# Performance work log

Hardware: AMD Instinct MI355X
Metric: run time of the kernel (lower is better)

Reference implementation:

```python
import jax, jax.numpy as jnp
import numpy as np

NUM_HEADS = 12
ROPE_THETA = 10000.0


def _rope_cos_sin(n, hd, dtype):
    inv_freq = 1.0 / (ROPE_THETA ** (np.arange(0, hd, 2, dtype=np.float64) / hd))
    freqs = np.outer(np.arange(n, dtype=np.float64), inv_freq)  # (N, hd/2)
    emb = np.concatenate([freqs, freqs], axis=-1)               # (N, hd)
    return jnp.asarray(np.cos(emb), dtype), jnp.asarray(np.sin(emb), dtype)


def _apply_rope(t, cos, sin):
    # t: (B, H, N, hd); rotate-half convention
    half = t.shape[-1] // 2
    t1, t2 = t[..., :half], t[..., half:]
    rot = jnp.concatenate([-t2, t1], axis=-1)
    return t * cos + rot * sin


def setup_inputs() -> dict:
    key = jax.random.key(0)
    k1, k2, k3 = jax.random.split(key, 3)
    B, N, C = 8, 1024, 768
    x = jax.random.normal(k1, (B, N, C), dtype=jnp.float32)
    w_qkv = jax.random.normal(k2, (C, 3 * C), dtype=jnp.float32) * 0.02
    w_proj = jax.random.normal(k3, (C, C), dtype=jnp.float32) * 0.02
    b_proj = jnp.zeros((C,), dtype=jnp.float32)
    return {"x": x, "w_qkv": w_qkv, "w_proj": w_proj, "b_proj": b_proj}


def reference(x, w_qkv, w_proj, b_proj):
    B, N, C = x.shape
    H = NUM_HEADS
    hd = C // H
    scale = hd ** -0.5
    # qkv: (B,N,3C) -> (B,N,3,H,hd) -> (B,H,3,N,hd)
    qkv = (x @ w_qkv).reshape(B, N, 3, H, hd).transpose(0, 3, 2, 1, 4)
    q, k, v = qkv[:, :, 0], qkv[:, :, 1], qkv[:, :, 2]  # each (B,H,N,hd)
    cos, sin = _rope_cos_sin(N, hd, x.dtype)
    q = _apply_rope(q, cos, sin)
    k = _apply_rope(k, cos, sin)
    attn = jax.nn.softmax(jnp.einsum("bhqd,bhkd->bhqk", q, k) * scale, axis=-1)
    out = jnp.einsum("bhqk,bhkd->bhqd", attn, v)  # (B,H,N,hd)
    out = out.transpose(0, 2, 1, 3).reshape(B, N, C)
    return out @ w_proj + b_proj
```

## Files before the change

kernel.cpp:

```cpp
#include <hip/hip_runtime.h>

typedef unsigned short ushort_t;
typedef __bf16 bf16x8 __attribute__((ext_vector_type(8)));
typedef float f32x4 __attribute__((ext_vector_type(4)));
typedef unsigned short u16x8 __attribute__((ext_vector_type(8)));
typedef unsigned int u32x2 __attribute__((ext_vector_type(2)));

#define MFMA16(a, b, c) __builtin_amdgcn_mfma_f32_16x16x32_bf16((a), (b), (c), 0, 0, 0)

#define SEQ 1024
#define NHEAD 12
#define HD 64
#define CDIM 768
#define TS 6291456
#define QSCALE 0.1803368801111204f

__device__ __forceinline__ ushort_t f2bf(float f) {
  __bf16 b = (__bf16)f;
  return __builtin_bit_cast(ushort_t, b);
}
__device__ __forceinline__ unsigned pk2(float lo, float hi) {
  return (unsigned)f2bf(lo) | ((unsigned)f2bf(hi) << 16);
}
__device__ __forceinline__ float bf2f(ushort_t h) {
  return __builtin_bit_cast(float, ((unsigned int)h) << 16);
}

typedef __attribute__((address_space(1))) void gvoid_t;
typedef __attribute__((address_space(3))) void lvoid_t;
__device__ __forceinline__ void async16(const ushort_t* g, ushort_t* l) {
  __builtin_amdgcn_global_load_lds((gvoid_t*)g, (lvoid_t*)l, 16, 0, 0);
}

__device__ __forceinline__ void transpose_body(const float* __restrict__ in,
                                               ushort_t* __restrict__ out,
                                               int R, int C, int bxi, int byi,
                                               float (*tile)[33]) {
  int bx = bxi * 32, by = byi * 32;
  int tx = threadIdx.x & 31, ty = threadIdx.x >> 5;
#pragma unroll
  for (int i = ty; i < 32; i += 8) {
    int r = by + i, c = bx + tx;
    if (r < R && c < C) tile[i][tx] = in[(size_t)r * C + c];
  }
  __syncthreads();
#pragma unroll
  for (int i = ty; i < 32; i += 8) {
    int r = bx + i, c = by + tx;
    if (r < C && c < R) out[(size_t)r * R + c] = f2bf(tile[tx][i]);
  }
}

__global__ void __launch_bounds__(256) prep_all(const float* __restrict__ x,
                                                const float* __restrict__ w_qkv,
                                                const float* __restrict__ w_proj,
                                                ushort_t* __restrict__ xb,
                                                ushort_t* __restrict__ wqkvT,
                                                ushort_t* __restrict__ wprojT,
                                                float* __restrict__ tab) {
  __shared__ float tile[32][33];
  const int bid = blockIdx.x;
  if (bid < 3072) {
    int i = (bid * 256 + threadIdx.x) * 8;
    float4 a = *(const float4*)(x + i);
    float4 b = *(const float4*)(x + i + 4);
    u16x8 r;
    r[0] = f2bf(a.x); r[1] = f2bf(a.y); r[2] = f2bf(a.z); r[3] = f2bf(a.w);
    r[4] = f2bf(b.x); r[5] = f2bf(b.y); r[6] = f2bf(b.z); r[7] = f2bf(b.w);
    *(u16x8*)(xb + i) = r;
  } else if (bid < 3072 + 1728) {
    int t = bid - 3072;
    transpose_body(w_qkv, wqkvT, 768, 2304, t % 72, t / 72, tile);
  } else if (bid < 3072 + 1728 + 576) {
    int t = bid - (3072 + 1728);
    transpose_body(w_proj, wprojT, 768, 768, t % 24, t / 24, tile);
  } else {
    int g = (bid - 5376) * 256 + threadIdx.x;
    int n = g >> 5, j = g & 31;
    double invf = pow(10000.0, -((double)(2 * j)) / 64.0);
    double fr = (double)n * invf;
    tab[g * 2]     = (float)cos(fr);
    tab[g * 2 + 1] = (float)sin(fr);
  }
}

__device__ __forceinline__ void gemm_bt_core(const ushort_t* __restrict__ A,
                                             const ushort_t* __restrict__ Bt,
                                             int K, int bm, int bn,
                                             ushort_t* ldsA, ushort_t* ldsB,
                                             f32x4 acc[4][4]) {
  const int tid = threadIdx.x;
  const int lane = tid & 63, wid = tid >> 6;
  const int wm = (wid >> 1) * 64, wn = (wid & 1) * 64;
  const int fr = lane & 15, fq = lane >> 4;
#pragma unroll
  for (int i = 0; i < 4; ++i)
#pragma unroll
    for (int j = 0; j < 4; ++j) acc[i][j] = (f32x4){0.f, 0.f, 0.f, 0.f};

  const int srow = tid >> 2;
  const int scol = (tid & 3) * 8;
  const size_t aOff = (size_t)(bm + srow) * K + scol;
  const size_t bOff = (size_t)(bn + srow) * K + scol;

  for (int kt = 0; kt < K; kt += 32) {
    async16(A + aOff + kt, ldsA + tid * 8);
    async16(A + aOff + (size_t)64 * K + kt, ldsA + 2048 + tid * 8);
    async16(Bt + bOff + kt, ldsB + tid * 8);
    async16(Bt + bOff + (size_t)64 * K + kt, ldsB + 2048 + tid * 8);
    __syncthreads();
    bf16x8 aF[4], bF[4];
#pragma unroll
    for (int i = 0; i < 4; ++i)
      aF[i] = *(const bf16x8*)(ldsA + (wm + i * 16 + fr) * 32 + fq * 8);
#pragma unroll
    for (int j = 0; j < 4; ++j)
      bF[j] = *(const bf16x8*)(ldsB + (wn + j * 16 + fr) * 32 + fq * 8);
#pragma unroll
    for (int i = 0; i < 4; ++i)
#pragma unroll
      for (int j = 0; j < 4; ++j) acc[i][j] = MFMA16(aF[i], bF[j], acc[i][j]);
    __syncthreads();
  }
}

__global__ void __launch_bounds__(256) gemm_qkv(const ushort_t* __restrict__ A,
                                                const ushort_t* __restrict__ Bt,
                                                const float* __restrict__ tab,
                                                ushort_t* __restrict__ qkv) {
  __shared__ __attribute__((aligned(16))) ushort_t ldsA[4096];
  __shared__ __attribute__((aligned(16))) ushort_t ldsB[4096];
  f32x4 acc[4][4];
  const int bm = blockIdx.y * 128, bn = blockIdx.x * 128;
  gemm_bt_core(A, Bt, CDIM, bm, bn, ldsA, ldsB, acc);
  const int lane = threadIdx.x & 63, wid = threadIdx.x >> 6;
  const int wm = (wid >> 1) * 64, wn = (wid & 1) * 64;
  const int fr = lane & 15, fq = lane >> 4;
  const int tensor = bn / 768;

  if (tensor < 2) {
    ushort_t* dstT = qkv + (size_t)tensor * TS;
    const float qs = (tensor == 0) ? QSCALE : 1.0f;
#pragma unroll
    for (int i = 0; i < 4; ++i) {
#pragma unroll
      for (int jp = 0; jp < 2; ++jp) {
        const int col = bn + wn + jp * 16 + fr;
        const int rem = col - tensor * 768;
        const int h = rem >> 6;
        const int d2 = rem & 31;
#pragma unroll
        for (int rr = 0; rr < 4; ++rr) {
          const int row = bm + wm + i * 16 + fq * 4 + rr;
          const int b = row >> 10, n = row & 1023;
          const float2 cs = ((const float2*)tab)[n * 32 + d2];
          const float av = acc[i][jp][rr], bv = acc[i][jp + 2][rr];
          const float o1 = (av * cs.x - bv * cs.y) * qs;
          const float o2 = (bv * cs.x + av * cs.y) * qs;
          ushort_t* dst = dstT + ((size_t)(b * NHEAD + h) * SEQ + n) * HD + d2;
          dst[0]  = f2bf(o1);
          dst[32] = f2bf(o2);
        }
      }
    }
  } else {
    ushort_t* vt = qkv + 2 * (size_t)TS;
#pragma unroll
    for (int i = 0; i < 4; ++i) {
      const int row0 = bm + wm + i * 16 + fq * 4;
      const int b = row0 >> 10, n0 = row0 & 1023;
#pragma unroll
      for (int j = 0; j < 4; ++j) {
        const int col = bn + wn + j * 16 + fr;
        const int rem = col - 1536;
        const int h = rem >> 6, d = rem & 63;
        u32x2 pk;
        pk[0] = pk2(acc[i][j][0], acc[i][j][1]);
        pk[1] = pk2(acc[i][j][2], acc[i][j][3]);
        *(u32x2*)(vt + ((size_t)(b * NHEAD + h) * HD + d) * SEQ + n0) = pk;
      }
    }
  }
}

__global__ void __launch_bounds__(256) gemm_proj(const ushort_t* __restrict__ A,
                                                 const ushort_t* __restrict__ Bt,
                                                 const float* __restrict__ bias,
                                                 float* __restrict__ Cout) {
  __shared__ __attribute__((aligned(16))) ushort_t ldsA[4096];
  __shared__ __attribute__((aligned(16))) ushort_t ldsB[4096];
  f32x4 acc[4][4];
  const int bm = blockIdx.y * 128, bn = blockIdx.x * 128;
  gemm_bt_core(A, Bt, CDIM, bm, bn, ldsA, ldsB, acc);
  const int lane = threadIdx.x & 63, wid = threadIdx.x >> 6;
  const int wm = (wid >> 1) * 64, wn = (wid & 1) * 64;
  const int fr = lane & 15, fq = lane >> 4;
#pragma unroll
  for (int i = 0; i < 4; ++i) {
#pragma unroll
    for (int j = 0; j < 4; ++j) {
      const int col = bn + wn + j * 16 + fr;
      const float bv = bias[col];
#pragma unroll
      for (int rr = 0; rr < 4; ++rr) {
        const int row = bm + wm + i * 16 + fq * 4 + rr;
        Cout[(size_t)row * CDIM + col] = acc[i][j][rr] + bv;
      }
    }
  }
}

__global__ void __launch_bounds__(256, 3) attn_fused(const ushort_t* __restrict__ Qb,
                                                     const ushort_t* __restrict__ Kb,
                                                     const ushort_t* __restrict__ VTb,
                                                     ushort_t* __restrict__ Ob) {
  __shared__ __attribute__((aligned(16))) ushort_t ldsK[2][2][2048];
  __shared__ __attribute__((aligned(16))) ushort_t ldsV[2][2][2048];
  __shared__ __attribute__((aligned(16))) ushort_t Pl[4][32 * 72];

  const int tid = threadIdx.x, lane = tid & 63, wid = tid >> 6;
  const int fr = lane & 15, fq = lane >> 4;

  const int f = blockIdx.x;
  const int xp = f & 7, rest = f >> 3;
  const int g = rest % 12, qb = rest / 12;
  const int head = g * 8 + xp;
  const int q0 = qb * 128;

  const ushort_t* Qh  = Qb  + (size_t)head * (SEQ * HD);
  const ushort_t* Kh  = Kb  + (size_t)head * (SEQ * HD);
  const ushort_t* VTh = VTb + (size_t)head * (HD * SEQ);

  bf16x8 qF[2][2];
#pragma unroll
  for (int qt = 0; qt < 2; ++qt) {
    const int qrow = q0 + wid * 32 + qt * 16 + fr;
    qF[qt][0] = *(const bf16x8*)(Qh + (size_t)qrow * HD + fq * 8);
    qF[qt][1] = *(const bf16x8*)(Qh + (size_t)qrow * HD + 32 + fq * 8);
  }

  f32x4 ot[2][4];
#pragma unroll
  for (int qt = 0; qt < 2; ++qt)
#pragma unroll
    for (int dt = 0; dt < 4; ++dt) ot[qt][dt] = (f32x4){0.f, 0.f, 0.f, 0.f};
  float lsum[2] = {0.f, 0.f};

  const int srow = tid >> 2;
  const int sc = (tid & 3) * 8;

#define STAGE(buf, kt)                                                          \
  {                                                                             \
    const ushort_t* ksrc = Kh + (size_t)((kt) * 64 + srow) * HD + sc;           \
    async16(ksrc,      &ldsK[buf][0][tid * 8]);                                 \
    async16(ksrc + 32, &ldsK[buf][1][tid * 8]);                                 \
    const ushort_t* vsrc = VTh + (size_t)srow * SEQ + (kt) * 64 + sc;           \
    async16(vsrc,      &ldsV[buf][0][tid * 8]);                                 \
    async16(vsrc + 32, &ldsV[buf][1][tid * 8]);                                 \
  }

  STAGE(0, 0);
  __syncthreads();

  for (int kt = 0; kt < 16; ++kt) {
    const int cur = kt & 1;
    if (kt < 15) STAGE(cur ^ 1, kt + 1);

    bf16x8 kf[4][2];
#pragma unroll
    for (int t = 0; t < 4; ++t)
#pragma unroll
      for (int ks = 0; ks < 2; ++ks)
        kf[t][ks] = *(const bf16x8*)&ldsK[cur][ks][(t * 16 + fr) * 32 + fq * 8];

    f32x4 st[2][4];
#pragma unroll
    for (int qt = 0; qt < 2; ++qt)
#pragma unroll
      for (int t = 0; t < 4; ++t) {
        f32x4 s = (f32x4){0.f, 0.f, 0.f, 0.f};
        s = MFMA16(kf[t][0], qF[qt][0], s);
        s = MFMA16(kf[t][1], qF[qt][1], s);
        st[qt][t] = s;
      }

    bf16x8 vf[4][2];
#pragma unroll
    for (int dt = 0; dt < 4; ++dt)
#pragma unroll
      for (int ks = 0; ks < 2; ++ks)
        vf[dt][ks] = *(const bf16x8*)&ldsV[cur][ks][(dt * 16 + fr) * 32 + fq * 8];

#pragma unroll
    for (int qt = 0; qt < 2; ++qt) {
      ushort_t* Pw = &Pl[wid][(qt * 16 + fr) * 72];
      float ls = lsum[qt];
#pragma unroll
      for (int t = 0; t < 4; ++t) {
        const float e0 = exp2f(st[qt][t][0]);
        const float e1 = exp2f(st[qt][t][1]);
        const float e2 = exp2f(st[qt][t][2]);
        const float e3 = exp2f(st[qt][t][3]);
        ls += (e0 + e1) + (e2 + e3);
        u32x2 pk;
        pk[0] = pk2(e0, e1);
        pk[1] = pk2(e2, e3);
        *(u32x2*)(Pw + t * 16 + fq * 4) = pk;
      }
      lsum[qt] = ls;
      bf16x8 pf0 = *(const bf16x8*)(Pw + fq * 8);
      bf16x8 pf1 = *(const bf16x8*)(Pw + 32 + fq * 8);
#pragma unroll
      for (int dt = 0; dt < 4; ++dt) {
        ot[qt][dt] = MFMA16(vf[dt][0], pf0, ot[qt][dt]);
        ot[qt][dt] = MFMA16(vf[dt][1], pf1, ot[qt][dt]);
      }
    }
    __syncthreads();
  }

  const int b = head / NHEAD, h = head - b * NHEAD;
#pragma unroll
  for (int qt = 0; qt < 2; ++qt) {
    float l = lsum[qt];
    l += __shfl_xor(l, 16);
    l += __shfl_xor(l, 32);
    const float inv = 1.0f / l;
    const int qrow = q0 + wid * 32 + qt * 16 + fr;
    ushort_t* obase = Ob + ((size_t)(b * SEQ + qrow)) * CDIM + h * HD;
#pragma unroll
    for (int dt = 0; dt < 4; ++dt) {
      u32x2 pk;
      pk[0] = pk2(ot[qt][dt][0] * inv, ot[qt][dt][1] * inv);
      pk[1] = pk2(ot[qt][dt][2] * inv, ot[qt][dt][3] * inv);
      *(u32x2*)(obase + dt * 16 + fq * 4) = pk;
    }
  }
}

extern "C" void kernel_launch(void* const* d_in, const int* in_sizes, int n_in,
                              void* d_out, int out_size, void* d_ws, size_t ws_size,
                              hipStream_t stream) {
  const float* x      = (const float*)d_in[0];
  const float* w_qkv  = (const float*)d_in[1];
  const float* w_proj = (const float*)d_in[2];
  const float* b_proj = (const float*)d_in[3];
  float* out = (float*)d_out;
  char* ws = (char*)d_ws;

  ushort_t* xb     = (ushort_t*)(ws + 0);
  ushort_t* wqkvT  = (ushort_t*)(ws + 12582912);
  ushort_t* wprojT = (ushort_t*)(ws + 16121856);
  ushort_t* qkv    = (ushort_t*)(ws + 17301504);
  float*    tab    = (float*)  (ws + 55050240);
  ushort_t* oattn  = (ushort_t*)(ws + 55312384);

  prep_all<<<5504, 256, 0, stream>>>(x, w_qkv, w_proj, xb, wqkvT, wprojT, tab);
  gemm_qkv<<<dim3(18, 64), 256, 0, stream>>>(xb, wqkvT, tab, qkv);
  attn_fused<<<768, 256, 0, stream>>>(qkv, qkv + TS, qkv + 2 * (size_t)TS, oattn);
  gemm_proj<<<dim3(6, 64), 256, 0, stream>>>(oattn, wprojT, b_proj, out);
}
```

Baseline: 220.6 us.

## Double-buffer GEMM LDS tiles and remap blocks for XCD-aware L2 locality

The shared GEMM core now uses two LDS buffers, so the async global-to-LDS loads for the next K-tile are issued while MFMAs run on the current tile, removing one barrier per iteration. Both GEMM kernels switch to a 1D grid with a swizzle that groups eight consecutive M-tiles onto the same XCD, so neighbouring blocks share A rows in L2. LDS use per block doubles to 32 KB, which could lower occupancy. The next-stage loads are issued without an explicit wait before the barrier, so correctness relies on __syncthreads draining outstanding global_load_lds operations.

```diff
diff --git a/kernel.cpp b/kernel.cpp
--- a/kernel.cpp
+++ b/kernel.cpp
@@ -21,9 +21,6 @@
 }
 __device__ __forceinline__ unsigned pk2(float lo, float hi) {
   return (unsigned)f2bf(lo) | ((unsigned)f2bf(hi) << 16);
-}
-__device__ __forceinline__ float bf2f(ushort_t h) {
-  return __builtin_bit_cast(float, ((unsigned int)h) << 16);
 }
 
 typedef __attribute__((address_space(1))) void gvoid_t;
@@ -87,7 +84,8 @@
 __device__ __forceinline__ void gemm_bt_core(const ushort_t* __restrict__ A,
                                              const ushort_t* __restrict__ Bt,
                                              int K, int bm, int bn,
-                                             ushort_t* ldsA, ushort_t* ldsB,
+                                             ushort_t (*ldsA)[4096],
+                                             ushort_t (*ldsB)[4096],
                                              f32x4 acc[4][4]) {
   const int tid = threadIdx.x;
   const int lane = tid & 63, wid = tid >> 6;
@@ -102,36 +100,51 @@
   const int scol = (tid & 3) * 8;
   const size_t aOff = (size_t)(bm + srow) * K + scol;
   const size_t bOff = (size_t)(bn + srow) * K + scol;
-
-  for (int kt = 0; kt < K; kt += 32) {
-    async16(A + aOff + kt, ldsA + tid * 8);
-    async16(A + aOff + (size_t)64 * K + kt, ldsA + 2048 + tid * 8);
-    async16(Bt + bOff + kt, ldsB + tid * 8);
-    async16(Bt + bOff + (size_t)64 * K + kt, ldsB + 2048 + tid * 8);
-    __syncthreads();
+  const int nIter = K >> 5;
+
+#define GSTAGE(buf, kt)                                                \
+  {                                                                    \
+    async16(A + aOff + (kt) * 32, ldsA[buf] + tid * 8);                \
+    async16(A + aOff + (size_t)64 * K + (kt) * 32,                     \
+            ldsA[buf] + 2048 + tid * 8);                               \
+    async16(Bt + bOff + (kt) * 32, ldsB[buf] + tid * 8);               \
+    async16(Bt + bOff + (size_t)64 * K + (kt) * 32,                    \
+            ldsB[buf] + 2048 + tid * 8);                               \
+  }
+
+  GSTAGE(0, 0);
+  __syncthreads();
+
+  for (int kt = 0; kt < nIter; ++kt) {
+    const int cur = kt & 1;
+    if (kt + 1 < nIter) GSTAGE(cur ^ 1, kt + 1);
     bf16x8 aF[4], bF[4];
 #pragma unroll
     for (int i = 0; i < 4; ++i)
-      aF[i] = *(const bf16x8*)(ldsA + (wm + i * 16 + fr) * 32 + fq * 8);
+      aF[i] = *(const bf16x8*)(ldsA[cur] + (wm + i * 16 + fr) * 32 + fq * 8);
 #pragma unroll
     for (int j = 0; j < 4; ++j)
-      bF[j] = *(const bf16x8*)(ldsB + (wn + j * 16 + fr) * 32 + fq * 8);
+      bF[j] = *(const bf16x8*)(ldsB[cur] + (wn + j * 16 + fr) * 32 + fq * 8);
 #pragma unroll
     for (int i = 0; i < 4; ++i)
 #pragma unroll
       for (int j = 0; j < 4; ++j) acc[i][j] = MFMA16(aF[i], bF[j], acc[i][j]);
     __syncthreads();
   }
+#undef GSTAGE
 }
 
 __global__ void __launch_bounds__(256) gemm_qkv(const ushort_t* __restrict__ A,
                                                 const ushort_t* __restrict__ Bt,
                                                 const float* __restrict__ tab,
                                                 ushort_t* __restrict__ qkv) {
-  __shared__ __attribute__((aligned(16))) ushort_t ldsA[4096];
-  __shared__ __attribute__((aligned(16))) ushort_t ldsB[4096];
+  __shared__ __attribute__((aligned(16))) ushort_t ldsA[2][4096];
+  __shared__ __attribute__((aligned(16))) ushort_t ldsB[2][4096];
   f32x4 acc[4][4];
-  const int bm = blockIdx.y * 128, bn = blockIdx.x * 128;
+  const int f = blockIdx.x;
+  const int xcd = f & 7, r = f >> 3;
+  const int bm = (xcd * 8 + (r & 7)) * 128;
+  const int bn = (r >> 3) * 128;
   gemm_bt_core(A, Bt, CDIM, bm, bn, ldsA, ldsB, acc);
   const int lane = threadIdx.x & 63, wid = threadIdx.x >> 6;
   const int wm = (wid >> 1) * 64, wn = (wid & 1) * 64;
@@ -187,10 +200,13 @@
                                                  const ushort_t* __restrict__ Bt,
                                                  const float* __restrict__ bias,
                                                  float* __restrict__ Cout) {
-  __shared__ __attribute__((aligned(16))) ushort_t ldsA[4096];
-  __shared__ __attribute__((aligned(16))) ushort_t ldsB[4096];
+  __shared__ __attribute__((aligned(16))) ushort_t ldsA[2][4096];
+  __shared__ __attribute__((aligned(16))) ushort_t ldsB[2][4096];
   f32x4 acc[4][4];
-  const int bm = blockIdx.y * 128, bn = blockIdx.x * 128;
+  const int f = blockIdx.x;
+  const int xcd = f & 7, r = f >> 3;
+  const int bm = (xcd * 8 + (r & 7)) * 128;
+  const int bn = (r >> 3) * 128;
   gemm_bt_core(A, Bt, CDIM, bm, bn, ldsA, ldsB, acc);
   const int lane = threadIdx.x & 63, wid = threadIdx.x >> 6;
   const int wm = (wid >> 1) * 64, wn = (wid & 1) * 64;
@@ -356,7 +372,7 @@
   ushort_t* oattn  = (ushort_t*)(ws + 55312384);
 
   prep_all<<<5504, 256, 0, stream>>>(x, w_qkv, w_proj, xb, wqkvT, wprojT, tab);
-  gemm_qkv<<<dim3(18, 64), 256, 0, stream>>>(xb, wqkvT, tab, qkv);
+  gemm_qkv<<<1152, 256, 0, stream>>>(xb, wqkvT, tab, qkv);
   attn_fused<<<768, 256, 0, stream>>>(qkv, qkv + TS, qkv + 2 * (size_t)TS, oattn);
-  gemm_proj<<<dim3(6, 64), 256, 0, stream>>>(oattn, wprojT, b_proj, out);
-}
+  gemm_proj<<<384, 256, 0, stream>>>(oattn, wprojT, b_proj, out);
+}
```

After: 225.2 us. 1.02x slower.
